# Kernel optimization log

Measured on AMD Instinct MI355X. Metric: run time of the kernel, lower is better.

## Reference

```python
import jax, jax.numpy as jnp
import numpy as np

N_KNOTS = 10
NC = 32
BATCH = 32
EPS = 1e-5

def _spline_matrix(n):
    step = 1.0 / (n - 1.0)
    mat = 4 * np.eye(n - 2)
    np.fill_diagonal(mat[1:, :-1], 1)
    np.fill_diagonal(mat[:-1, 1:], 1)
    A = 6 * np.linalg.inv(mat) / step ** 2
    z = np.zeros(n - 2)
    A = np.vstack([z, A, z])            # [n, n-2]
    B = np.zeros((n - 2, n))
    np.fill_diagonal(B, 1)
    np.fill_diagonal(B[:, 1:], -2)
    np.fill_diagonal(B[:, 2:], 1)
    return np.dot(A, B).astype(np.float32)  # [n, n]

def setup_inputs() -> dict:
    key = jax.random.key(0)
    ks = jax.random.split(key, 8)
    n, nc = N_KNOTS, NC
    inp = {}
    inp['batch'] = jax.random.uniform(ks[0], (BATCH, 3, 256, 256), dtype=jnp.float32)
    chans = [3, nc, 2 * nc, 4 * nc, 8 * nc, 16 * nc]
    for i in range(5):
        ci, co = chans[i], chans[i + 1]
        inp['c%d_w' % (i + 1)] = jax.random.normal(jax.random.fold_in(ks[1], i), (co, ci, 3, 3), dtype=jnp.float32) * 0.1
        inp['c%d_b' % (i + 1)] = jnp.zeros((co,), jnp.float32)
        inp['bn%d_g' % (i + 1)] = jnp.ones((co,), jnp.float32)
        inp['bn%d_b' % (i + 1)] = jnp.zeros((co,), jnp.float32)
    inp['l1_w'] = jax.random.normal(ks[2], (100 * n, 16 * nc * 7 * 7), dtype=jnp.float32) * 0.02
    inp['l1_b'] = jnp.zeros((100 * n,), jnp.float32)
    inp['l2_w'] = jax.random.normal(ks[3], (3 * n, 100 * n), dtype=jnp.float32) * 0.02
    inp['l2_b'] = jnp.zeros((3 * n,), jnp.float32)
    inp['matrix'] = jnp.asarray(_spline_matrix(n))
    return inp

def _conv_bn(x, w, b, g, be):
    # conv (stride 2, VALID) -> relu -> batchnorm (training-mode batch stats)
    y = jax.lax.conv_general_dilated(x, w, (2, 2), 'VALID', dimension_numbers=('NCHW', 'OIHW', 'NCHW'))
    y = jax.nn.relu(y + b[None, :, None, None])
    m = jnp.mean(y, axis=(0, 2, 3))
    v = jnp.var(y, axis=(0, 2, 3))
    inv = jax.lax.rsqrt(v + EPS)
    return g[None, :, None, None] * (y - m[None, :, None, None]) * inv[None, :, None, None] + be[None, :, None, None]

def _forward(batch, c1_w, c1_b, bn1_g, bn1_b, c2_w, c2_b, bn2_g, bn2_b,
             c3_w, c3_b, bn3_g, bn3_b, c4_w, c4_b, bn4_g, bn4_b,
             c5_w, c5_b, bn5_g, bn5_b, l1_w, l1_b, l2_w, l2_b, matrix):
    n = matrix.shape[0]
    h = 1.0 / (n - 1.0)  # knot spacing (self.step)
    B, _, H, W = batch.shape

    x = _conv_bn(batch, c1_w, c1_b, bn1_g, bn1_b)
    x = _conv_bn(x, c2_w, c2_b, bn2_g, bn2_b)
    x = _conv_bn(x, c3_w, c3_b, bn3_g, bn3_b)
    x = _conv_bn(x, c4_w, c4_b, bn4_g, bn4_b)
    x = _conv_bn(x, c5_w, c5_b, bn5_g, bn5_b)
    x = x.reshape(B, -1)
    x = jax.nn.relu(x @ l1_w.T + l1_b)
    x = x @ l2_w.T + l2_b
    ys = x.reshape(B, 3, n) / 100.0

    identity = jnp.arange(n, dtype=batch.dtype) / (n - 1)
    ys_aug = ys + identity                                    # [B,3,n]
    # second-derivative values M at knots (natural cubic spline solve as dense matmul)
    M = jnp.einsum('ij,bcj->bci', matrix, ys_aug)             # [B,3,n]
    a = (M[..., 1:] - M[..., :-1]) / (6 * h)                  # [B,3,n-1]
    b_ = M[..., :-1] / 2
    c_ = (ys_aug[..., 1:] - ys_aug[..., :-1]) / h - (M[..., 1:] + 2 * M[..., :-1]) * (h / 6)
    d_ = ys_aug[..., :-1]

    def eval_spline(xv):  # xv: [B,3,K] -> [B,3,K]; gather segment coeffs instead of one-hot matmul
        xi = jnp.clip(jnp.floor(xv / h), 0, n - 2).astype(jnp.int32)
        xf = xv - xi.astype(xv.dtype) * h
        ag = jnp.take_along_axis(a, xi, axis=-1)
        bg = jnp.take_along_axis(b_, xi, axis=-1)
        cg = jnp.take_along_axis(c_, xi, axis=-1)
        dg = jnp.take_along_axis(d_, xi, axis=-1)
        return ((ag * xf + bg) * xf + cg) * xf + dg

    out = eval_spline(batch.reshape(B, 3, H * W)).reshape(B, 3, H, W)
    vals = jnp.arange(255, dtype=batch.dtype) / 255.0          # arange(0,1,1/255)
    splines = eval_spline(jnp.broadcast_to(vals, (B, 3, 255)))
    return out, splines

def reference(batch, c1_w, c1_b, bn1_g, bn1_b, c2_w, c2_b, bn2_g, bn2_b,
              c3_w, c3_b, bn3_g, bn3_b, c4_w, c4_b, bn4_g, bn4_b,
              c5_w, c5_b, bn5_g, bn5_b, l1_w, l1_b, l2_w, l2_b, matrix):
    return _forward(batch, c1_w, c1_b, bn1_g, bn1_b, c2_w, c2_b, bn2_g, bn2_b,
                    c3_w, c3_b, bn3_g, bn3_b, c4_w, c4_b, bn4_g, bn4_b,
                    c5_w, c5_b, bn5_g, bn5_b, l1_w, l1_b, l2_w, l2_b, matrix)
```

## Files before the change

### kernel.cpp

```cpp
#include <hip/hip_runtime.h>
#include <hip/hip_bf16.h>

#define BEPS 1e-5f
#define FC1_KS 98
#define FC1_KC 256
#define C1NB 2017
#define STS 512

typedef __attribute__((ext_vector_type(8))) short short8v;
typedef __attribute__((ext_vector_type(4))) float f32x4;
typedef unsigned short ushort_t;

__device__ __forceinline__ float bf2f(ushort_t u) {
    unsigned int x = ((unsigned int)u) << 16;
    return __builtin_bit_cast(float, x);
}
__device__ __forceinline__ ushort_t f2bf(float v) {
    __hip_bfloat16 h = __float2bfloat16(v);
    return *(ushort_t*)&h;
}

__global__ __launch_bounds__(256) void conv1_direct(
    const float* __restrict__ in, const float* __restrict__ w,
    const float* __restrict__ bias, ushort_t* __restrict__ out) {
    __shared__ float ws[864];
    __shared__ float bs[32];
    const int tid = threadIdx.x;
    for (int i = tid; i < 864; i += 256) ws[i] = w[i];
    if (tid < 32) bs[tid] = bias[tid];
    __syncthreads();

    const int TOT = 32 * 16129;
    int p = blockIdx.x * 256 + tid;
    if (p >= TOT) return;
    int b = p / 16129, pp = p - b * 16129;
    int i = pp / 127, j = pp - i * 127;
    const float* ib = in + ((long long)b * 3) * 65536 + (2 * i) * 256 + 2 * j;
    float patch[27];
#pragma unroll
    for (int ci = 0; ci < 3; ++ci)
#pragma unroll
        for (int di = 0; di < 3; ++di) {
            const float* rp = ib + ci * 65536 + di * 256;
            float2 v01 = *(const float2*)rp;
            patch[ci * 9 + di * 3 + 0] = v01.x;
            patch[ci * 9 + di * 3 + 1] = v01.y;
            patch[ci * 9 + di * 3 + 2] = rp[2];
        }

    ushort_t res[32];
#pragma unroll
    for (int co = 0; co < 32; co += 4) {
        float a0 = bs[co], a1 = bs[co + 1], a2 = bs[co + 2], a3 = bs[co + 3];
#pragma unroll
        for (int t = 0; t < 27; ++t) {
            float pv = patch[t];
            a0 = fmaf(pv, ws[(co + 0) * 27 + t], a0);
            a1 = fmaf(pv, ws[(co + 1) * 27 + t], a1);
            a2 = fmaf(pv, ws[(co + 2) * 27 + t], a2);
            a3 = fmaf(pv, ws[(co + 3) * 27 + t], a3);
        }
        res[co + 0] = f2bf(fmaxf(a0, 0.f));
        res[co + 1] = f2bf(fmaxf(a1, 0.f));
        res[co + 2] = f2bf(fmaxf(a2, 0.f));
        res[co + 3] = f2bf(fmaxf(a3, 0.f));
    }
    ushort_t* ob = out + (long long)p * 32;
#pragma unroll
    for (int v = 0; v < 4; ++v)
        *(short8v*)&ob[v * 8] = *(const short8v*)&res[v * 8];
}

__global__ __launch_bounds__(256) void conv_mfma(
    const ushort_t* __restrict__ in, const ushort_t* __restrict__ wf,
    const float* __restrict__ effb, ushort_t* __restrict__ out,
    float* __restrict__ pacc,
    int B, int Ci, int lgCi, int Hi, int Wi, int Co, int Ho, int Wo,
    int K, int Kp, int kcount) {
    const int HoWo = Ho * Wo;
    const int N = B * HoWo;
    __shared__ __align__(16) ushort_t As[64 * 64];
    __shared__ __align__(16) ushort_t Bs[128 * 64];
    const int tid = threadIdx.x;
    const int m0 = blockIdx.y * 64;
    const int n0 = blockIdx.x * 128;
    const int kbeg = blockIdx.z * kcount;

    const int rowA = tid >> 2;
    const int kqA = (tid & 3) * 16;
    const ushort_t* wrowA = wf + (long long)(m0 + rowA) * Kp + kbeg + kqA;
    const int swA = (rowA & 7) << 3;
    const int rowB = tid >> 1;
    const int kqB = (tid & 1) * 32;
    const int n = n0 + rowB;
    const int nn = (n < N) ? n : (N - 1);
    const int pb = nn / HoWo, pp = nn - pb * HoWo;
    const int pi = pp / Wo, pj = pp - pi * Wo;
    const long long base0 = ((long long)pb * Hi + 2 * pi) * Wi + 2 * pj;
    const int swB = (rowB & 7) << 3;

    const int w = tid >> 6;
    const int lane = tid & 63;
    const int wco = (w >> 1) * 32, wpx = (w & 1) * 64;
    const int lm = lane & 15, lk = lane >> 4;

    f32x4 acc[2][4] = {};
    for (int k0 = 0; k0 < kcount; k0 += 64) {
        {
            short8v a0 = *(const short8v*)(wrowA + k0);
            short8v a1 = *(const short8v*)(wrowA + k0 + 8);
            *(short8v*)&As[rowA * 64 + ((kqA + 0) ^ swA)] = a0;
            *(short8v*)&As[rowA * 64 + ((kqA + 8) ^ swA)] = a1;
        }
#pragma unroll
        for (int ch = 0; ch < 2; ++ch) {
            int c16 = kqB + ch * 16;
            int kg = kbeg + k0 + c16;
            int tap = kg >> lgCi;
            tap = tap > 8 ? 8 : tap;
            int ci0 = kg & (Ci - 1);
            int dy = tap / 3, dx = tap - dy * 3;
            const ushort_t* src = in + (base0 + dy * Wi + dx) * Ci + ci0;
            short8v v0 = *(const short8v*)src;
            short8v v1 = *(const short8v*)(src + 8);
            *(short8v*)&Bs[rowB * 64 + ((c16 + 0) ^ swB)] = v0;
            *(short8v*)&Bs[rowB * 64 + ((c16 + 8) ^ swB)] = v1;
        }
        __syncthreads();
#pragma unroll
        for (int kk = 0; kk < 2; ++kk) {
            const int kb = kk * 32 + lk * 8;
            const int ra0 = wco + lm, ra1 = wco + 16 + lm;
            short8v a0 = *(const short8v*)&As[ra0 * 64 + (kb ^ ((ra0 & 7) << 3))];
            short8v a1 = *(const short8v*)&As[ra1 * 64 + (kb ^ ((ra1 & 7) << 3))];
            const int rb0 = wpx + lm, rb1 = wpx + 16 + lm;
            const int rb2 = wpx + 32 + lm, rb3 = wpx + 48 + lm;
            short8v b0 = *(const short8v*)&Bs[rb0 * 64 + (kb ^ ((rb0 & 7) << 3))];
            short8v b1 = *(const short8v*)&Bs[rb1 * 64 + (kb ^ ((rb1 & 7) << 3))];
            short8v b2 = *(const short8v*)&Bs[rb2 * 64 + (kb ^ ((rb2 & 7) << 3))];
            short8v b3 = *(const short8v*)&Bs[rb3 * 64 + (kb ^ ((rb3 & 7) << 3))];
            acc[0][0] = __builtin_amdgcn_mfma_f32_16x16x32_bf16(a0, b0, acc[0][0], 0, 0, 0);
            acc[0][1] = __builtin_amdgcn_mfma_f32_16x16x32_bf16(a0, b1, acc[0][1], 0, 0, 0);
            acc[0][2] = __builtin_amdgcn_mfma_f32_16x16x32_bf16(a0, b2, acc[0][2], 0, 0, 0);
            acc[0][3] = __builtin_amdgcn_mfma_f32_16x16x32_bf16(a0, b3, acc[0][3], 0, 0, 0);
            acc[1][0] = __builtin_amdgcn_mfma_f32_16x16x32_bf16(a1, b0, acc[1][0], 0, 0, 0);
            acc[1][1] = __builtin_amdgcn_mfma_f32_16x16x32_bf16(a1, b1, acc[1][1], 0, 0, 0);
            acc[1][2] = __builtin_amdgcn_mfma_f32_16x16x32_bf16(a1, b2, acc[1][2], 0, 0, 0);
            acc[1][3] = __builtin_amdgcn_mfma_f32_16x16x32_bf16(a1, b3, acc[1][3], 0, 0, 0);
        }
        __syncthreads();
    }
    if (pacc) {
        float* pbuf = pacc + ((long long)blockIdx.z * N) * Co;
#pragma unroll
        for (int nb = 0; nb < 4; ++nb) {
            int np = n0 + wpx + nb * 16 + lm;
            if (np >= N) continue;
#pragma unroll
            for (int amr = 0; amr < 2; ++amr) {
                int cobase = m0 + wco + amr * 16 + lk * 4;
                float4 vv = make_float4(acc[amr][nb][0], acc[amr][nb][1],
                                        acc[amr][nb][2], acc[amr][nb][3]);
                *(float4*)&pbuf[(long long)np * Co + cobase] = vv;
            }
        }
    } else {
#pragma unroll
        for (int nb = 0; nb < 4; ++nb) {
            int np = n0 + wpx + nb * 16 + lm;
            if (np >= N) continue;
#pragma unroll
            for (int amr = 0; amr < 2; ++amr) {
                int cobase = m0 + wco + amr * 16 + lk * 4;
                float4 eb = *(const float4*)&effb[cobase];
                ushort4 u;
                u.x = f2bf(fmaxf(acc[amr][nb][0] + eb.x, 0.f));
                u.y = f2bf(fmaxf(acc[amr][nb][1] + eb.y, 0.f));
                u.z = f2bf(fmaxf(acc[amr][nb][2] + eb.z, 0.f));
                u.w = f2bf(fmaxf(acc[amr][nb][3] + eb.w, 0.f));
                *(ushort4*)&out[(long long)np * Co + cobase] = u;
            }
        }
    }
}

__global__ void convz_reduce(const float* __restrict__ pacc, const float* __restrict__ effb,
                             ushort_t* __restrict__ out, int N, int Co, int lgCo, int Z,
                             int total) {
    int idx = blockIdx.x * 256 + threadIdx.x;
    if (idx >= total) return;
    int c = idx & (Co - 1);
    float s = effb[c];
    for (int z = 0; z < Z; ++z) s += pacc[((long long)z * N << lgCo) + idx];
    out[idx] = f2bf(fmaxf(s, 0.f));
}

__global__ __launch_bounds__(256) void stats_flat(
    const ushort_t* __restrict__ y, float* __restrict__ part,
    long long total, int C, int S) {
    const int tid = threadIdx.x;
    float sum[8] = {}, sq[8] = {};
    const long long nchunk = (total + 2047) >> 11;
    for (long long g = blockIdx.x; g < nchunk; g += S) {
        long long off = (g << 11) + tid * 8;
        if (off + 8 <= total) {
            short8v v8 = *(const short8v*)(y + off);
#pragma unroll
            for (int j = 0; j < 8; ++j) {
                float v = bf2f((ushort_t)v8[j]);
                sum[j] += v;
                sq[j] = fmaf(v, v, sq[j]);
            }
        }
    }
    __shared__ float rs[256][8], rq[256][8];
#pragma unroll
    for (int j = 0; j < 8; ++j) { rs[tid][j] = sum[j]; rq[tid][j] = sq[j]; }
    __syncthreads();
    const int G = C >> 3;
    const int TPG = 256 / G;
    for (int c = tid; c < C; c += 256) {
        int grp = c >> 3, j = c & 7;
        float s = 0.f, q = 0.f;
        for (int i = 0; i < TPG; ++i) {
            s += rs[grp + i * G][j];
            q += rq[grp + i * G][j];
        }
        part[(c * S + blockIdx.x) * 2 + 0] = s;
        part[(c * S + blockIdx.x) * 2 + 1] = q;
    }
}

__global__ __launch_bounds__(256) void stats_final_w(
    const float* __restrict__ part, const float* __restrict__ g,
    const float* __restrict__ be, float* __restrict__ scale,
    float* __restrict__ shift, int C, int S, float invN) {
    int c = blockIdx.x * 4 + (threadIdx.x >> 6);
    int lane = threadIdx.x & 63;
    if (c >= C) return;
    float s = 0.f, q = 0.f;
    for (int i = lane; i < S; i += 64) {
        s += part[(c * S + i) * 2 + 0];
        q += part[(c * S + i) * 2 + 1];
    }
#pragma unroll
    for (int off = 32; off > 0; off >>= 1) {
        s += __shfl_down(s, off, 64);
        q += __shfl_down(q, off, 64);
    }
    if (lane == 0) {
        float m = s * invN;
        float v = q * invN - m * m;
        float inv = rsqrtf(v + BEPS);
        float sc = g[c] * inv;
        scale[c] = sc;
        shift[c] = be[c] - m * sc;
    }
}

__global__ __launch_bounds__(256) void fold_fused(
    const float* __restrict__ w, const float* __restrict__ scale,
    const float* __restrict__ shift, const float* __restrict__ bias,
    ushort_t* __restrict__ wout, float* __restrict__ effb,
    int Ci, int lgCi, int K, int Kp, int Co, int WB) {
    if ((int)blockIdx.x < WB) {
        int idx = blockIdx.x * 256 + threadIdx.x;
        if (idx >= Co * Kp) return;
        int co = idx / Kp, k = idx - co * Kp;
        ushort_t o = 0;
        if (k < K) {
            int tap = k >> lgCi;
            int ci = k & (Ci - 1);
            o = f2bf(w[((long long)co * Ci + ci) * 9 + tap] * scale[ci]);
        }
        wout[idx] = o;
    } else {
        int co = ((int)blockIdx.x - WB) * 4 + (threadIdx.x >> 6);
        int lane = threadIdx.x & 63;
        if (co >= Co) return;
        const int CK = Ci * 9;
        const float* wr = w + (long long)co * CK;
        float acc = 0.f;
        for (int k = lane; k < CK; k += 64) acc = fmaf(wr[k], shift[k / 9], acc);
#pragma unroll
        for (int off = 32; off > 0; off >>= 1) acc += __shfl_down(acc, off, 64);
        if (lane == 0) effb[co] = acc + bias[co];
    }
}

__global__ void bn_apply_x(const ushort_t* __restrict__ y, const float* __restrict__ scale,
                           const float* __restrict__ shift, ushort_t* __restrict__ xB) {
    int idx = blockIdx.x * blockDim.x + threadIdx.x;
    if (idx >= 802816) return;
    int b = idx / 25088, k = idx - b * 25088;
    int c = k / 49, p = k - c * 49;
    float v = bf2f(y[((long long)b * 49 + p) * 512 + c]);
    xB[idx] = f2bf(fmaf(v, scale[c], shift[c]));
}

__global__ __launch_bounds__(256) void fc1_mfma(
    const float* __restrict__ w, const ushort_t* __restrict__ xB,
    float* __restrict__ part) {
    const int K = 25088;
    __shared__ __align__(16) ushort_t As[64 * 256];
    __shared__ __align__(16) ushort_t Bs[32 * 256];
    const int tid = threadIdx.x;
    const int m0 = blockIdx.y * 64;
    const int kbeg = blockIdx.x * FC1_KC;

    {
        const int r = tid >> 2;
        const int kq = (tid & 3) * 64;
        const int m = m0 + r;
        const bool mv = (m < 1000);
        const float* wr = w + (long long)m * K + kbeg + kq;
        const int sw = (r & 7) << 3;
#pragma unroll
        for (int g = 0; g < 8; ++g) {
            short8v o = {0, 0, 0, 0, 0, 0, 0, 0};
            if (mv) {
                float4 f0 = *(const float4*)(wr + g * 8);
                float4 f1 = *(const float4*)(wr + g * 8 + 4);
                o[0] = (short)f2bf(f0.x); o[1] = (short)f2bf(f0.y);
                o[2] = (short)f2bf(f0.z); o[3] = (short)f2bf(f0.w);
                o[4] = (short)f2bf(f1.x); o[5] = (short)f2bf(f1.y);
                o[6] = (short)f2bf(f1.z); o[7] = (short)f2bf(f1.w);
            }
            *(short8v*)&As[r * 256 + ((kq + g * 8) ^ sw)] = o;
        }
    }
    {
        const int b = tid >> 3;
        const int kq = (tid & 7) * 32;
        const ushort_t* xr = xB + (long long)b * K + kbeg + kq;
        const int sw = (b & 7) << 3;
#pragma unroll
        for (int g = 0; g < 4; ++g) {
            short8v v = *(const short8v*)(xr + g * 8);
            *(short8v*)&Bs[b * 256 + ((kq + g * 8) ^ sw)] = v;
        }
    }
    __syncthreads();
    const int wv = tid >> 6, lane = tid & 63;
    const int lm = lane & 15, lk = lane >> 4;
    const int wm = wv * 16;
    f32x4 acc0 = {}, acc1 = {};
    const int ra = wm + lm;
    const int swa = (ra & 7) << 3;
    const int swb = (lm & 7) << 3;
#pragma unroll
    for (int s = 0; s < 8; ++s) {
        int kb = s * 32 + lk * 8;
        short8v av = *(const short8v*)&As[ra * 256 + (kb ^ swa)];
        short8v b0 = *(const short8v*)&Bs[lm * 256 + (kb ^ swb)];
        short8v b1 = *(const short8v*)&Bs[(16 + lm) * 256 + (kb ^ swb)];
        acc0 = __builtin_amdgcn_mfma_f32_16x16x32_bf16(av, b0, acc0, 0, 0, 0);
        acc1 = __builtin_amdgcn_mfma_f32_16x16x32_bf16(av, b1, acc1, 0, 0, 0);
    }
    float* pb = part + ((long long)blockIdx.y * FC1_KS + blockIdx.x) * 2048;
#pragma unroll
    for (int r = 0; r < 4; ++r) {
        pb[(wm + lk * 4 + r) * 32 + lm] = acc0[r];
        pb[(wm + lk * 4 + r) * 32 + 16 + lm] = acc1[r];
    }
}

__global__ void fc1_reduce(const float* __restrict__ part, const float* __restrict__ bias,
                           float* __restrict__ z) {
    int idx = blockIdx.x * blockDim.x + threadIdx.x;
    if (idx >= 32000) return;
    int o = idx >> 5, b = idx & 31;
    int mt = o >> 6, mr = o & 63;
    const float* p = part + ((long long)mt * FC1_KS) * 2048 + mr * 32 + b;
    float s0 = 0.f, s1 = 0.f;
    int ks = 0;
    for (; ks + 1 < FC1_KS; ks += 2) {
        s0 += p[(long long)ks * 2048];
        s1 += p[(long long)(ks + 1) * 2048];
    }
    for (; ks < FC1_KS; ++ks) s0 += p[(long long)ks * 2048];
    z[b * 1000 + o] = fmaxf(s0 + s1 + bias[o], 0.f);
}

__global__ __launch_bounds__(256) void fc2_v2(const float* __restrict__ z,
                                              const float* __restrict__ w,
                                              const float* __restrict__ bias,
                                              float* __restrict__ ys) {
    int gid = blockIdx.x * 4 + (threadIdx.x >> 6);
    int lane = threadIdx.x & 63;
    if (gid >= 960) return;
    int b = gid / 30, o = gid - b * 30;
    const float* zr = z + (long long)b * 1000;
    const float* wr = w + (long long)o * 1000;
    float acc = 0.f;
    for (int k = lane; k < 1000; k += 64) acc = fmaf(zr[k], wr[k], acc);
    for (int off = 32; off > 0; off >>= 1) acc += __shfl_down(acc, off, 64);
    if (lane == 0) ys[gid] = acc + bias[o];
}

__global__ void spline_coeff(const float* __restrict__ ysraw, const float* __restrict__ matrix,
                             float4* __restrict__ coef) {
    int r = threadIdx.x;
    if (r >= 96) return;
    const float h = 1.0f / 9.0f;
    float ya[10];
    int b = r / 3, ch = r % 3;
#pragma unroll
    for (int j = 0; j < 10; ++j)
        ya[j] = ysraw[b * 30 + ch * 10 + j] / 100.0f + (float)j / 9.0f;
    float M[10];
#pragma unroll
    for (int i = 0; i < 10; ++i) {
        float acc = 0.f;
#pragma unroll
        for (int j = 0; j < 10; ++j) acc = fmaf(matrix[i * 10 + j], ya[j], acc);
        M[i] = acc;
    }
#pragma unroll
    for (int k = 0; k < 9; ++k) {
        float a = (M[k + 1] - M[k]) / (6.0f * h);
        float bb = M[k] * 0.5f;
        float cc = (ya[k + 1] - ya[k]) / h - (M[k + 1] + 2.0f * M[k]) * (h / 6.0f);
        float dd = ya[k];
        coef[r * 9 + k] = make_float4(a, bb, cc, dd);
    }
}

__global__ void eval_all(const float4* __restrict__ batch4, const float4* __restrict__ coef,
                         float4* __restrict__ out4, float* __restrict__ outt) {
    int idx = blockIdx.x * blockDim.x + threadIdx.x;
    const float h = 1.0f / 9.0f;
    if (idx < 1572864) {
        int plane = idx >> 14;
        float4 xv4 = batch4[idx];
        float xin[4] = {xv4.x, xv4.y, xv4.z, xv4.w};
        float xout[4];
#pragma unroll
        for (int e = 0; e < 4; ++e) {
            float xv = xin[e];
            int xi = (int)floorf(xv / h);
            xi = min(max(xi, 0), 8);
            float xf = xv - (float)xi * h;
            float4 cf = coef[plane * 9 + xi];
            xout[e] = fmaf(fmaf(fmaf(cf.x, xf, cf.y), xf, cf.z), xf, cf.w);
        }
        out4[idx] = make_float4(xout[0], xout[1], xout[2], xout[3]);
    } else {
        int t = idx - 1572864;
        if (t >= 96 * 255) return;
        int plane = t / 255;
        int j = t - plane * 255;
        float xv = (float)j / 255.0f;
        int xi = (int)floorf(xv / h);
        xi = min(max(xi, 0), 8);
        float xf = xv - (float)xi * h;
        float4 cf = coef[plane * 9 + xi];
        outt[t] = fmaf(fmaf(fmaf(cf.x, xf, cf.y), xf, cf.z), xf, cf.w);
    }
}

extern "C" void kernel_launch(void* const* d_in, const int* in_sizes, int n_in,
                              void* d_out, int out_size, void* d_ws, size_t ws_size,
                              hipStream_t stream) {
    const int B = 32;
    const float* batch = (const float*)d_in[0];
    const float* cw[5] = {(const float*)d_in[1], (const float*)d_in[5], (const float*)d_in[9],
                          (const float*)d_in[13], (const float*)d_in[17]};
    const float* cb[5] = {(const float*)d_in[2], (const float*)d_in[6], (const float*)d_in[10],
                          (const float*)d_in[14], (const float*)d_in[18]};
    const float* bg[5] = {(const float*)d_in[3], (const float*)d_in[7], (const float*)d_in[11],
                          (const float*)d_in[15], (const float*)d_in[19]};
    const float* bb[5] = {(const float*)d_in[4], (const float*)d_in[8], (const float*)d_in[12],
                          (const float*)d_in[16], (const float*)d_in[20]};
    const float* l1w = (const float*)d_in[21];
    const float* l1b = (const float*)d_in[22];
    const float* l2w = (const float*)d_in[23];
    const float* l2b = (const float*)d_in[24];
    const float* matrix = (const float*)d_in[25];

    float* f = (float*)d_ws;
    const size_t A_F = 8258048;
    const size_t Bq_F = 4064256;
    const size_t W_F = 589824;
    ushort_t* bufA = (ushort_t*)f;
    ushort_t* bufB = (ushort_t*)(f + A_F);
    ushort_t* Wf_bf = (ushort_t*)(f + A_F + Bq_F);
    float* effb  = f + A_F + Bq_F + W_F;
    float* scale = effb + 512;
    float* shift = scale + 512;
    float* part  = shift + 512;
    float* x5    = part + 524288;
    float* pacc  = x5 + 802816;
    float* z1    = pacc + 3686400;
    float* ysb   = z1 + 32000;
    float4* coef = (float4*)(ysb + 960);

    const int Ci[5]   = {3, 32, 64, 128, 256};
    const int lgCi[5] = {0, 5, 6, 7, 8};
    const int Co[5]   = {32, 64, 128, 256, 512};
    const int Hi[5]   = {256, 127, 63, 31, 15};
    const int Ho[5]   = {127, 63, 31, 15, 7};
    const int Zl[5]   = {1, 1, 1, 2, 3};

    ushort_t* bufs[2] = {bufA, bufB};

    conv1_direct<<<C1NB, 256, 0, stream>>>(batch, cw[0], cb[0], bufA);
    {
        long long total = (long long)B * 16129 * 32;
        stats_flat<<<STS, 256, 0, stream>>>(bufA, part, total, 32, STS);
        stats_final_w<<<8, 256, 0, stream>>>(part, bg[0], bb[0], scale, shift, 32, STS,
                                             32.0f / (float)total);
    }

    const ushort_t* cur = bufA;
    for (int l = 1; l < 5; ++l) {
        ushort_t* outb = bufs[l % 2];
        int K = Ci[l] * 9;
        int Kp = (K + 63) & ~63;
        int WB = (Co[l] * Kp + 255) / 256;
        int BBk = (Co[l] + 3) / 4;
        fold_fused<<<WB + BBk, 256, 0, stream>>>(cw[l], scale, shift, cb[l], Wf_bf, effb,
                                                 Ci[l], lgCi[l], K, Kp, Co[l], WB);
        int N = B * Ho[l] * Ho[l];
        int Z = Zl[l];
        int kcount = Kp / Z;
        dim3 grid((N + 127) / 128, Co[l] / 64, Z);
        if (Z == 1) {
            conv_mfma<<<grid, 256, 0, stream>>>(cur, Wf_bf, effb, outb, nullptr,
                                                B, Ci[l], lgCi[l], Hi[l], Hi[l], Co[l],
                                                Ho[l], Ho[l], K, Kp, kcount);
        } else {
            conv_mfma<<<grid, 256, 0, stream>>>(cur, Wf_bf, effb, nullptr, pacc,
                                                B, Ci[l], lgCi[l], Hi[l], Hi[l], Co[l],
                                                Ho[l], Ho[l], K, Kp, kcount);
            int total = N * Co[l];
            int lgCo = (Co[l] == 256) ? 8 : 9;
            convz_reduce<<<(total + 255) / 256, 256, 0, stream>>>(pacc, effb, outb,
                                                                  N, Co[l], lgCo, Z, total);
        }
        long long total = (long long)N * Co[l];
        stats_flat<<<STS, 256, 0, stream>>>(outb, part, total, Co[l], STS);
        stats_final_w<<<(Co[l] + 3) / 4, 256, 0, stream>>>(part, bg[l], bb[l], scale, shift,
                                                           Co[l], STS, (float)Co[l] / (float)total);
        cur = outb;
    }

    ushort_t* xB = (ushort_t*)x5;
    bn_apply_x<<<(802816 + 255) / 256, 256, 0, stream>>>(cur, scale, shift, xB);
    {
        dim3 grid(FC1_KS, 16);
        fc1_mfma<<<grid, 256, 0, stream>>>(l1w, xB, pacc);
    }
    fc1_reduce<<<(32000 + 255) / 256, 256, 0, stream>>>(pacc, l1b, z1);
    fc2_v2<<<240, 256, 0, stream>>>(z1, l2w, l2b, ysb);
    spline_coeff<<<1, 96, 0, stream>>>(ysb, matrix, coef);

    float* out = (float*)d_out;
    int evtot = 1572864 + 96 * 255;
    eval_all<<<(evtot + 255) / 256, 256, 0, stream>>>((const float4*)batch, coef,
                                                      (float4*)out, out + 6291456);
}
```

Before: 258.7 us.

## Fuse batchnorm statistics into conv epilogue and split-K reduction kernels

Conv layers without a split-K pass now compute per-channel sums and sums of squares in the MFMA epilogue. They reduce these across lanes with shuffles and shared memory and write per-block partials, so the separate stats_flat pass that re-read the bf16 activations is gone. Split-K layers replace convz_reduce plus stats_flat with a single convz_stats kernel that sums the partials, applies bias and ReLU, writes bf16 and accumulates statistics in one pass. This saves launches and a full activation read per layer, at the cost of extra epilogue work, a block-wide sync and more shared memory in the conv kernel.

After: 245.8 us. -5.0%, faster.

```diff
diff --git a/kernel.cpp b/kernel.cpp
--- a/kernel.cpp
+++ b/kernel.cpp
@@ -74,9 +74,9 @@
 __global__ __launch_bounds__(256) void conv_mfma(
     const ushort_t* __restrict__ in, const ushort_t* __restrict__ wf,
     const float* __restrict__ effb, ushort_t* __restrict__ out,
-    float* __restrict__ pacc,
+    float* __restrict__ pacc, float* __restrict__ spart,
     int B, int Ci, int lgCi, int Hi, int Wi, int Co, int Ho, int Wo,
-    int K, int Kp, int kcount) {
+    int K, int Kp, int kcount, int Spart) {
     const int HoWo = Ho * Wo;
     const int N = B * HoWo;
     __shared__ __align__(16) ushort_t As[64 * 64];
@@ -165,34 +165,115 @@
             }
         }
     } else {
+        float ssum[2][4] = {}, ssq[2][4] = {};
 #pragma unroll
         for (int nb = 0; nb < 4; ++nb) {
             int np = n0 + wpx + nb * 16 + lm;
-            if (np >= N) continue;
+            bool val = (np < N);
 #pragma unroll
             for (int amr = 0; amr < 2; ++amr) {
                 int cobase = m0 + wco + amr * 16 + lk * 4;
                 float4 eb = *(const float4*)&effb[cobase];
-                ushort4 u;
-                u.x = f2bf(fmaxf(acc[amr][nb][0] + eb.x, 0.f));
-                u.y = f2bf(fmaxf(acc[amr][nb][1] + eb.y, 0.f));
-                u.z = f2bf(fmaxf(acc[amr][nb][2] + eb.z, 0.f));
-                u.w = f2bf(fmaxf(acc[amr][nb][3] + eb.w, 0.f));
-                *(ushort4*)&out[(long long)np * Co + cobase] = u;
+                float v0 = fmaxf(acc[amr][nb][0] + eb.x, 0.f);
+                float v1 = fmaxf(acc[amr][nb][1] + eb.y, 0.f);
+                float v2 = fmaxf(acc[amr][nb][2] + eb.z, 0.f);
+                float v3 = fmaxf(acc[amr][nb][3] + eb.w, 0.f);
+                if (val) {
+                    ushort4 u;
+                    u.x = f2bf(v0); u.y = f2bf(v1); u.z = f2bf(v2); u.w = f2bf(v3);
+                    *(ushort4*)&out[(long long)np * Co + cobase] = u;
+                    ssum[amr][0] += v0; ssq[amr][0] = fmaf(v0, v0, ssq[amr][0]);
+                    ssum[amr][1] += v1; ssq[amr][1] = fmaf(v1, v1, ssq[amr][1]);
+                    ssum[amr][2] += v2; ssq[amr][2] = fmaf(v2, v2, ssq[amr][2]);
+                    ssum[amr][3] += v3; ssq[amr][3] = fmaf(v3, v3, ssq[amr][3]);
+                }
             }
         }
-    }
-}
-
-__global__ void convz_reduce(const float* __restrict__ pacc, const float* __restrict__ effb,
-                             ushort_t* __restrict__ out, int N, int Co, int lgCo, int Z,
-                             int total) {
-    int idx = blockIdx.x * 256 + threadIdx.x;
-    if (idx >= total) return;
-    int c = idx & (Co - 1);
-    float s = effb[c];
-    for (int z = 0; z < Z; ++z) s += pacc[((long long)z * N << lgCo) + idx];
-    out[idx] = f2bf(fmaxf(s, 0.f));
+#pragma unroll
+        for (int mm = 1; mm < 16; mm <<= 1) {
+#pragma unroll
+            for (int amr = 0; amr < 2; ++amr)
+#pragma unroll
+                for (int r = 0; r < 4; ++r) {
+                    ssum[amr][r] += __shfl_xor(ssum[amr][r], mm, 64);
+                    ssq[amr][r] += __shfl_xor(ssq[amr][r], mm, 64);
+                }
+        }
+        __shared__ float lss[4][32], lsq[4][32];
+        if (lm == 0) {
+#pragma unroll
+            for (int amr = 0; amr < 2; ++amr)
+#pragma unroll
+                for (int r = 0; r < 4; ++r) {
+                    lss[w][amr * 16 + lk * 4 + r] = ssum[amr][r];
+                    lsq[w][amr * 16 + lk * 4 + r] = ssq[amr][r];
+                }
+        }
+        __syncthreads();
+        if (tid < 64) {
+            int half = tid >> 5, c32 = tid & 31;
+            float s = lss[half * 2][c32] + lss[half * 2 + 1][c32];
+            float q = lsq[half * 2][c32] + lsq[half * 2 + 1][c32];
+            int c = m0 + half * 32 + c32;
+            spart[((long long)c * Spart + blockIdx.x) * 2 + 0] = s;
+            spart[((long long)c * Spart + blockIdx.x) * 2 + 1] = q;
+        }
+    }
+}
+
+__global__ __launch_bounds__(256) void convz_stats(
+    const float* __restrict__ pacc, const float* __restrict__ effb,
+    ushort_t* __restrict__ out, float* __restrict__ part,
+    long long total, int Co, int Z) {
+    const int tid = threadIdx.x;
+    const int c0 = (tid * 8) & (Co - 1);
+    float eb[8];
+    {
+        float4 e0 = *(const float4*)&effb[c0];
+        float4 e1 = *(const float4*)&effb[c0 + 4];
+        eb[0] = e0.x; eb[1] = e0.y; eb[2] = e0.z; eb[3] = e0.w;
+        eb[4] = e1.x; eb[5] = e1.y; eb[6] = e1.z; eb[7] = e1.w;
+    }
+    float sum[8] = {}, sq[8] = {};
+    const long long nchunk = total >> 11;
+    for (long long g = blockIdx.x; g < nchunk; g += 512) {
+        long long off = (g << 11) + tid * 8;
+        float v[8];
+#pragma unroll
+        for (int j = 0; j < 8; ++j) v[j] = eb[j];
+        for (int z = 0; z < Z; ++z) {
+            const float* pz = pacc + (long long)z * total + off;
+            float4 a = *(const float4*)pz;
+            float4 b2 = *(const float4*)(pz + 4);
+            v[0] += a.x; v[1] += a.y; v[2] += a.z; v[3] += a.w;
+            v[4] += b2.x; v[5] += b2.y; v[6] += b2.z; v[7] += b2.w;
+        }
+        short8v o;
+#pragma unroll
+        for (int j = 0; j < 8; ++j) {
+            float r = fmaxf(v[j], 0.f);
+            o[j] = (short)f2bf(r);
+            sum[j] += r;
+            sq[j] = fmaf(r, r, sq[j]);
+        }
+        *(short8v*)&out[off] = o;
+    }
+    __shared__ float rs[256][8], rq[256][8];
+#pragma unroll
+    for (int j = 0; j < 8; ++j) { rs[tid][j] = sum[j]; rq[tid][j] = sq[j]; }
+    __syncthreads();
+    const int G = Co >> 3;
+    const int TPG = 256 / G;
+    for (int c = tid; c < Co; c += 256) {
+        int grp = c >> 3, j = c & 7;
+        float s = 0.f, q = 0.f;
+        for (int i = 0; i < TPG; ++i) {
+            s += rs[grp + i * G][j];
+            q += rq[grp + i * G][j];
+        }
+        part[(c * 512 + blockIdx.x) * 2 + 0] = s;
+        part[(c * 512 + blockIdx.x) * 2 + 1] = q;
+    }
 }
 
 __global__ __launch_bounds__(256) void stats_flat(
@@ -240,8 +321,8 @@
     if (c >= C) return;
     float s = 0.f, q = 0.f;
     for (int i = lane; i < S; i += 64) {
-        s += part[(c * S + i) * 2 + 0];
-        q += part[(c * S + i) * 2 + 1];
+        s += part[((long long)c * S + i) * 2 + 0];
+        q += part[((long long)c * S + i) * 2 + 1];
     }
 #pragma unroll
     for (int off = 32; off > 0; off >>= 1) {
@@ -509,7 +590,7 @@
         long long total = (long long)B * 16129 * 32;
         stats_flat<<<STS, 256, 0, stream>>>(bufA, part, total, 32, STS);
         stats_final_w<<<8, 256, 0, stream>>>(part, bg[0], bb[0], scale, shift, 32, STS,
-                                             32.0f / (float)total);
+                                             1.0f / (float)(B * 16129));
     }
 
     const ushort_t* cur = bufA;
@@ -526,22 +607,20 @@
         int kcount = Kp / Z;
         dim3 grid((N + 127) / 128, Co[l] / 64, Z);
         if (Z == 1) {
-            conv_mfma<<<grid, 256, 0, stream>>>(cur, Wf_bf, effb, outb, nullptr,
+            conv_mfma<<<grid, 256, 0, stream>>>(cur, Wf_bf, effb, outb, nullptr, part,
                                                 B, Ci[l], lgCi[l], Hi[l], Hi[l], Co[l],
-                                                Ho[l], Ho[l], K, Kp, kcount);
+                                                Ho[l], Ho[l], K, Kp, kcount, grid.x);
+            stats_final_w<<<(Co[l] + 3) / 4, 256, 0, stream>>>(
+                part, bg[l], bb[l], scale, shift, Co[l], grid.x, 1.0f / (float)N);
         } else {
-            conv_mfma<<<grid, 256, 0, stream>>>(cur, Wf_bf, effb, nullptr, pacc,
+            conv_mfma<<<grid, 256, 0, stream>>>(cur, Wf_bf, effb, nullptr, pacc, nullptr,
                                                 B, Ci[l], lgCi[l], Hi[l], Hi[l], Co[l],
-                                                Ho[l], Ho[l], K, Kp, kcount);
-            int total = N * Co[l];
-            int lgCo = (Co[l] == 256) ? 8 : 9;
-            convz_reduce<<<(total + 255) / 256, 256, 0, stream>>>(pacc, effb, outb,
-                                                                  N, Co[l], lgCo, Z, total);
-        }
-        long long total = (long long)N * Co[l];
-        stats_flat<<<STS, 256, 0, stream>>>(outb, part, total, Co[l], STS);
-        stats_final_w<<<(Co[l] + 3) / 4, 256, 0, stream>>>(part, bg[l], bb[l], scale, shift,
-                                                           Co[l], STS, (float)Co[l] / (float)total);
+                                                Ho[l], Ho[l], K, Kp, kcount, 0);
+            long long total = (long long)N * Co[l];
+            convz_stats<<<512, 256, 0, stream>>>(pacc, effb, outb, part, total, Co[l], Z);
+            stats_final_w<<<(Co[l] + 3) / 4, 256, 0, stream>>>(
+                part, bg[l], bb[l], scale, shift, Co[l], 512, 1.0f / (float)N);
+        }
         cur = outb;
     }
 
```
